# Kernel tuning notes

Measured on AMD Instinct MI355X. Metric: run time of the kernel, lower is better.

## Reference

```python
import jax, jax.numpy as jnp
import numpy as np

NUM_HEADS = 4

def setup_inputs() -> dict:
    key = jax.random.key(0)
    ks = jax.random.split(key, 5)
    B, T, F, C = 2, 128, 256, 256
    # weights scaled ~1/sqrt(C) so softmax is not saturated
    s = 1.0 / np.sqrt(C)
    return {
        "x": jax.random.normal(ks[0], (B, T, F, C), jnp.float32),
        "w_in": jax.random.normal(ks[1], (3 * C, C), jnp.float32) * s,
        "b_in": jax.random.normal(ks[2], (3 * C,), jnp.float32) * 0.01,
        "w_out": jax.random.normal(ks[3], (C, C), jnp.float32) * s,
        "b_out": jax.random.normal(ks[4], (C,), jnp.float32) * 0.01,
        "band": 16,
    }

def reference(x, w_in, b_in, w_out, b_out, band):
    B, T, F, C = x.shape
    H = NUM_HEADS
    D = C // H
    x2 = x.reshape(B * T, F, C)  # attention over frequency, independent per (B,T)
    qkv = x2 @ w_in.T + b_in  # [BT, F, 3C]
    q, k, v = jnp.split(qkv, 3, axis=-1)
    def heads(t):
        return t.reshape(B * T, F, H, D).transpose(0, 2, 1, 3)  # [BT, H, F, D]
    q, k, v = heads(q), heads(k), heads(v)
    scores = jnp.einsum('bhid,bhjd->bhij', q, k) / jnp.sqrt(jnp.asarray(D, x.dtype))
    i = jnp.arange(F)[:, None]
    j = jnp.arange(F)[None, :]
    keep = jnp.abs(i - j) <= band  # banded locality mask [F, F]
    scores = jnp.where(keep, scores, -jnp.inf)
    attn = jax.nn.softmax(scores, axis=-1)
    out = jnp.einsum('bhij,bhjd->bhid', attn, v)  # [BT, H, F, D]
    out = out.transpose(0, 2, 1, 3).reshape(B * T, F, C)
    y = out @ w_out.T + b_out
    return y.reshape(B, T, F, C)
```

## Files before the change

### kernel.cpp

```cpp
#include <hip/hip_runtime.h>
#include <hip/hip_bf16.h>
#include <cstdint>

typedef unsigned int u32;
typedef __attribute__((ext_vector_type(8))) __bf16 bf16x8;
typedef __attribute__((ext_vector_type(4))) float f32x4;
typedef __attribute__((ext_vector_type(2))) _Float16 half2_t;
typedef __attribute__((ext_vector_type(4))) _Float16 half4;
typedef __attribute__((ext_vector_type(2))) __fp16 fp16x2;

#define BT_N 256
#define F_N 256
#define C_N 256
#define H_N 4
#define D_N 64
#define TC_N 768
#define M_N (BT_N * F_N)
#define VT_ST 268

__device__ __forceinline__ ushort f2bf(float f) {
  u32 u = __float_as_uint(f);
  u32 r = (u + 0x7fffu + ((u >> 16) & 1u)) >> 16;
  return (ushort)r;
}

__device__ __forceinline__ u32 pkbf(float a, float b) {
  return (u32)f2bf(a) | ((u32)f2bf(b) << 16);
}

__device__ __forceinline__ void gload_lds16(const ushort* g, ushort* l) {
  __builtin_amdgcn_global_load_lds(
      (const __attribute__((address_space(1))) u32*)g,
      (__attribute__((address_space(3))) u32*)l, 16, 0, 0);
}

__global__ __launch_bounds__(256) void cvt2_f32_bf16_k(
    const float* __restrict__ s0, ushort* __restrict__ d0, int n0,
    const float* __restrict__ s1, ushort* __restrict__ d1, int n1) {
  int idx = blockIdx.x * 256 + threadIdx.x;
  int stride = gridDim.x * 256;
  for (int i = idx; i < n0 + n1; i += stride) {
    const float4* s = (i < n0) ? ((const float4*)s0 + i) : ((const float4*)s1 + (i - n0));
    ushort* d = (i < n0) ? (d0 + (size_t)i * 4) : (d1 + (size_t)(i - n0) * 4);
    float4 v = *s;
    *(uint2*)d = make_uint2(pkbf(v.x, v.y), pkbf(v.z, v.w));
  }
}

template <bool AF32, typename OutT>
__global__ __launch_bounds__(256, 2) void gemm_bt(
    const void* __restrict__ Ap, const ushort* __restrict__ Bp,
    const float* __restrict__ bias, OutT* __restrict__ Cp,
    int N, int NTN, int nwg8) {
  constexpr bool F32OUT = (sizeof(OutT) == 4);
  constexpr int SMEM_BYTES = F32OUT ? 67584 : 65536;
  __shared__ char smem[SMEM_BYTES];
  ushort* smemH = (ushort*)smem;

  const int tid = threadIdx.x;
  const int lane = tid & 63;
  const int wid = tid >> 6;
  const int wr = wid >> 1, wc = wid & 1;
  const int l15 = lane & 15, l4 = lane >> 4;
  const int b = blockIdx.x;
  const int bid = (b & 7) * nwg8 + (b >> 3);
  const int tm = bid / NTN;
  const int tn = bid - tm * NTN;
  const int rowBase = tm * 128, colBase = tn * 128;

  f32x4 acc[4][4] = {};

  const int ar = (tid >> 3);
  const int c8 = tid & 7;
  const int akk = ((c8 ^ (ar & 7)) << 3);
  const ushort* gB = Bp + (size_t)(colBase + ar) * 256 + akk;
  const ushort* gAh = (const ushort*)Ap + (size_t)(rowBase + ar) * 256 + akk;
  const float* gAf = (const float*)Ap + (size_t)(rowBase + ar) * 256 + c8 * 8;

  float4 a0[4], a1[4];

#define STAGE_B(buf, k0)                                                      \
  {                                                                           \
    ushort* Bs_ = smemH + 16384 + (buf) * 8192;                               \
    _Pragma("unroll") for (int c = 0; c < 4; ++c)                             \
      gload_lds16(gB + (size_t)(c * 32) * 256 + (k0),                         \
                  Bs_ + (size_t)(c * 256 + (wid << 6)) * 8);                  \
  }
#define STAGE_A16(buf, k0)                                                    \
  {                                                                           \
    ushort* As_ = smemH + (buf) * 8192;                                       \
    _Pragma("unroll") for (int c = 0; c < 4; ++c)                             \
      gload_lds16(gAh + (size_t)(c * 32) * 256 + (k0),                        \
                  As_ + (size_t)(c * 256 + (wid << 6)) * 8);                  \
  }
#define LOAD_AF(k0)                                                           \
  {                                                                           \
    _Pragma("unroll") for (int c = 0; c < 4; ++c) {                           \
      const float* ga = gAf + (size_t)(c * 32) * 256 + (k0);                  \
      a0[c] = *(const float4*)ga;                                             \
      a1[c] = *(const float4*)(ga + 4);                                       \
    }                                                                         \
  }
#define WRITE_AF(buf)                                                         \
  {                                                                           \
    ushort* As_ = smemH + (buf) * 8192;                                       \
    _Pragma("unroll") for (int c = 0; c < 4; ++c) {                           \
      int row = ar + 32 * c;                                                  \
      u32 p0 = pkbf(a0[c].x, a0[c].y), p1 = pkbf(a0[c].z, a0[c].w);           \
      u32 p2 = pkbf(a1[c].x, a1[c].y), p3 = pkbf(a1[c].z, a1[c].w);           \
      *(uint4*)(As_ + row * 64 + ((c8 ^ (ar & 7)) * 8)) =                     \
          make_uint4(p0, p1, p2, p3);                                         \
    }                                                                         \
  }

  if constexpr (AF32) {
    LOAD_AF(0);
    STAGE_B(0, 0);
    WRITE_AF(0);
  } else {
    STAGE_A16(0, 0);
    STAGE_B(0, 0);
  }

  int cur = 0;
#pragma unroll
  for (int t = 0; t < 4; ++t) {
    __syncthreads();
    if (t < 3) {
      if constexpr (AF32) { LOAD_AF((t + 1) * 64); }
      else { STAGE_A16(cur ^ 1, (t + 1) * 64); }
      STAGE_B(cur ^ 1, (t + 1) * 64);
    }
    const ushort* As_ = smemH + cur * 8192;
    const ushort* Bs_ = smemH + 16384 + cur * 8192;
#pragma unroll
    for (int kk = 0; kk < 2; ++kk) {
      bf16x8 af[4];
      bf16x8 bfr[4];
#pragma unroll
      for (int i2 = 0; i2 < 4; ++i2) {
        int row = wr * 64 + i2 * 16 + l15;
        af[i2] = *(const bf16x8*)(As_ + row * 64 + (((kk * 4 + l4) ^ (l15 & 7)) * 8));
      }
#pragma unroll
      for (int j2 = 0; j2 < 4; ++j2) {
        int row = wc * 64 + j2 * 16 + l15;
        bfr[j2] = *(const bf16x8*)(Bs_ + row * 64 + (((kk * 4 + l4) ^ (l15 & 7)) * 8));
      }
#pragma unroll
      for (int i2 = 0; i2 < 4; ++i2)
#pragma unroll
        for (int j2 = 0; j2 < 4; ++j2)
          acc[i2][j2] = __builtin_amdgcn_mfma_f32_16x16x32_bf16(
              af[i2], bfr[j2], acc[i2][j2], 0, 0, 0);
    }
    if constexpr (AF32) {
      if (t < 3) WRITE_AF(cur ^ 1);
    }
    cur ^= 1;
  }
#undef STAGE_B
#undef STAGE_A16
#undef LOAD_AF
#undef WRITE_AF

  __syncthreads();
  if constexpr (F32OUT) {
    float* eb = (float*)smem;
#pragma unroll
    for (int j2 = 0; j2 < 4; ++j2) {
      float bv = bias[colBase + wc * 64 + j2 * 16 + l15];
#pragma unroll
      for (int i2 = 0; i2 < 4; ++i2)
#pragma unroll
        for (int r = 0; r < 4; ++r)
          eb[(wr * 64 + i2 * 16 + l4 * 4 + r) * 132 + wc * 64 + j2 * 16 + l15] =
              acc[i2][j2][r] + bv;
    }
    __syncthreads();
#pragma unroll
    for (int i = 0; i < 32; ++i) {
      int row = wid * 32 + i;
      uint2 d = *(const uint2*)((const u32*)eb + row * 132 + lane * 2);
      *(uint2*)((float*)Cp + (size_t)(rowBase + row) * N + colBase + lane * 2) = d;
    }
  } else {
    ushort* eb = smemH;
#pragma unroll
    for (int j2 = 0; j2 < 4; ++j2) {
      float bv = bias[colBase + wc * 64 + j2 * 16 + l15];
#pragma unroll
      for (int i2 = 0; i2 < 4; ++i2)
#pragma unroll
        for (int r = 0; r < 4; ++r) {
          _Float16 h = (_Float16)(acc[i2][j2][r] + bv);
          eb[(wr * 64 + i2 * 16 + l4 * 4 + r) * 136 + wc * 64 + j2 * 16 + l15] =
              __builtin_bit_cast(ushort, h);
        }
    }
    __syncthreads();
#pragma unroll
    for (int i = 0; i < 16; ++i) {
      int row = wid * 32 + 2 * i + (lane >> 5);
      int hl = lane & 31;
      uint2 d = *(const uint2*)(eb + row * 136 + hl * 4);
      *(uint2*)((_Float16*)Cp + (size_t)(rowBase + row) * N + colBase + hl * 4) = d;
    }
  }
}

__global__ __launch_bounds__(256) void attn_mfma(
    const _Float16* __restrict__ qkv, ushort* __restrict__ aout) {
  __shared__ ushort smem[18432 + 64 * VT_ST];
  const int tid = threadIdx.x;
  const int bt = blockIdx.x >> 2;
  const int h = blockIdx.x & 3;
  const _Float16* base = qkv + (size_t)bt * 256 * 768 + h * 64;
  ushort* klds = smem;
  ushort* vlds = smem + 18432;

  {
    const int r0 = tid >> 3, c8 = tid & 7;
#pragma unroll
    for (int p = 0; p < 8; ++p) {
      int j = p * 32 + r0;
      const uint4 k4 = *(const uint4*)(base + (size_t)j * 768 + 256 + c8 * 8);
      *(uint4*)(klds + j * 72 + c8 * 8) = k4;
      const uint4 v4 = *(const uint4*)(base + (size_t)j * 768 + 512 + c8 * 8);
      const ushort* vh = (const ushort*)&v4;
      ushort* vtp = vlds + (c8 * 8) * VT_ST + j;
#pragma unroll
      for (int i = 0; i < 8; ++i) vtp[i * VT_ST] = vh[i];
    }
  }

  const int w = tid >> 6, lane = tid & 63;
  const int l15 = lane & 15, g = lane >> 4, g4 = g * 4;

  uint2 qf0[4], qf1[4], qf2[4], qf3[4];
  {
    const uint2* q0 = (const uint2*)(base + (size_t)(w * 64 + 0 * 16 + l15) * 768 + g4);
    const uint2* q1 = (const uint2*)(base + (size_t)(w * 64 + 1 * 16 + l15) * 768 + g4);
    const uint2* q2 = (const uint2*)(base + (size_t)(w * 64 + 2 * 16 + l15) * 768 + g4);
    const uint2* q3 = (const uint2*)(base + (size_t)(w * 64 + 3 * 16 + l15) * 768 + g4);
#pragma unroll
    for (int ks = 0; ks < 4; ++ks) {
      qf0[ks] = q0[ks * 4]; qf1[ks] = q1[ks * 4];
      qf2[ks] = q2[ks * 4]; qf3[ks] = q3[ks * 4];
    }
  }

  u32 bb = 0;
#pragma unroll
  for (int jt = 0; jt < 3; ++jt)
#pragma unroll
    for (int r = 0; r < 4; ++r) {
      int d = 16 * jt + g4 + r - 16 - l15;
      if (d >= -16 && d <= 16) bb |= 1u << (jt * 4 + r);
    }

  __syncthreads();

  const float SC = 0.18033688f;

#pragma unroll
  for (int rt = 0; rt < 4; ++rt) {
    const int R0 = w * 64 + rt * 16;
    const int Jc = R0 - 16;
    const uint2* qf = (rt == 0) ? qf0 : (rt == 1) ? qf1 : (rt == 2) ? qf2 : qf3;

    f32x4 st[3] = {};
#pragma unroll
    for (int jt = 0; jt < 3; ++jt) {
      int krow = Jc + 16 * jt + l15;
      krow = krow < 0 ? 0 : (krow > 255 ? 255 : krow);
      const ushort* kp = klds + krow * 72 + g4;
#pragma unroll
      for (int ks = 0; ks < 4; ++ks) {
        uint2 kf = *(const uint2*)(kp + ks * 16);
        st[jt] = __builtin_amdgcn_mfma_f32_16x16x16f16(
            __builtin_bit_cast(half4, kf), __builtin_bit_cast(half4, qf[ks]),
            st[jt], 0, 0, 0);
      }
    }

    float l_acc = 0.f;
    float pp[3][4];
#pragma unroll
    for (int jt = 0; jt < 3; ++jt)
#pragma unroll
      for (int r = 0; r < 4; ++r) {
        int jg = Jc + 16 * jt + g4 + r;
        bool keep = (((bb >> (jt * 4 + r)) & 1u) != 0) && (jg >= 0) && (jg < 256);
        float pv = keep ? __builtin_amdgcn_exp2f(st[jt][r] * SC) : 0.f;
        pp[jt][r] = pv;
        l_acc += pv;
      }
    l_acc += __shfl_xor(l_acc, 16, 64);
    l_acc += __shfl_xor(l_acc, 32, 64);
    const float inv = 1.f / l_acc;

    uint2 pf[3];
#pragma unroll
    for (int jt = 0; jt < 3; ++jt) {
      fp16x2 a = __builtin_amdgcn_cvt_pkrtz(pp[jt][0] * inv, pp[jt][1] * inv);
      fp16x2 c = __builtin_amdgcn_cvt_pkrtz(pp[jt][2] * inv, pp[jt][3] * inv);
      pf[jt].x = __builtin_bit_cast(u32, a);
      pf[jt].y = __builtin_bit_cast(u32, c);
    }

    f32x4 ot[4] = {};
#pragma unroll
    for (int kt = 0; kt < 3; ++kt) {
      int jb = Jc + 16 * kt + g4;
      jb = jb < 0 ? 0 : (jb > 252 ? 252 : jb);
#pragma unroll
      for (int mt = 0; mt < 4; ++mt) {
        uint2 vfr = *(const uint2*)(vlds + (16 * mt + l15) * VT_ST + jb);
        ot[mt] = __builtin_amdgcn_mfma_f32_16x16x16f16(
            __builtin_bit_cast(half4, vfr), __builtin_bit_cast(half4, pf[kt]),
            ot[mt], 0, 0, 0);
      }
    }

    ushort* orow = aout + (size_t)(bt * 256 + R0 + l15) * 256 + h * 64 + g4;
#pragma unroll
    for (int mt = 0; mt < 4; ++mt) {
      u32 lo = (u32)f2bf(ot[mt][0]) | ((u32)f2bf(ot[mt][1]) << 16);
      u32 hi = (u32)f2bf(ot[mt][2]) | ((u32)f2bf(ot[mt][3]) << 16);
      *(uint2*)(orow + mt * 16) = make_uint2(lo, hi);
    }
  }
}

extern "C" void kernel_launch(void* const* d_in, const int* in_sizes, int n_in,
                              void* d_out, int out_size, void* d_ws, size_t ws_size,
                              hipStream_t stream) {
  const float* x = (const float*)d_in[0];
  const float* w_in = (const float*)d_in[1];
  const float* b_in = (const float*)d_in[2];
  const float* w_out = (const float*)d_in[3];
  const float* b_out = (const float*)d_in[4];
  float* y = (float*)d_out;

  char* ws = (char*)d_ws;
  const size_t qkv_bytes = (size_t)M_N * TC_N * 2;
  _Float16* qkv = (_Float16*)ws;
  ushort* attn = (ushort*)(ws + qkv_bytes);
  ushort* winb = attn + (size_t)M_N * C_N;
  ushort* woutb = winb + TC_N * C_N;

  cvt2_f32_bf16_k<<<256, 256, 0, stream>>>(w_in, winb, TC_N * C_N / 4,
                                           w_out, woutb, C_N * C_N / 4);

  gemm_bt<true, _Float16><<<(M_N / 128) * (TC_N / 128), 256, 0, stream>>>(
      x, winb, b_in, qkv, TC_N, TC_N / 128, (M_N / 128) * (TC_N / 128) / 8);

  attn_mfma<<<BT_N * H_N, 256, 0, stream>>>(qkv, attn);

  gemm_bt<false, float><<<(M_N / 128) * (C_N / 128), 256, 0, stream>>>(
      attn, woutb, b_out, y, C_N, C_N / 128, (M_N / 128) * (C_N / 128) / 8);
}
```

Before: 114.9 us.

## Add dedicated QKV GEMM keeping full-K x rows in registers

Replaces the generic tiled QKV projection with a kernel where each block owns 64 rows of x, loads and converts the full K=256 row slice to bf16 once into registers, and then loops over all six 128-column weight tiles, streaming weights through double-buffered LDS. This removes the redundant re-reading and re-conversion of fp32 x for each of the six N tiles, cutting global traffic on the largest input. In exchange each block does a longer serial loop with high register use (64 bf16x8 A fragments), which may lower occupancy, and the epilogue now writes fp16 output directly from MFMA layout without LDS staging.

```diff
diff --git a/kernel.cpp b/kernel.cpp
--- a/kernel.cpp
+++ b/kernel.cpp
@@ -47,6 +47,100 @@
   }
 }
 
+__global__ __launch_bounds__(256) void gemm_qkv(
+    const float* __restrict__ x, const ushort* __restrict__ wb,
+    const float* __restrict__ bias, _Float16* __restrict__ qkv, int nwg8) {
+  __shared__ ushort Bs[2][128 * 64];
+
+  const int tid = threadIdx.x;
+  const int lane = tid & 63;
+  const int wid = tid >> 6;
+  const int wr = wid >> 1, wc = wid & 1;
+  const int l15 = lane & 15, g = lane >> 4;
+  const int b = blockIdx.x;
+  const int bid = (b & 7) * nwg8 + (b >> 3);
+  const int rowBase = bid * 64;
+
+  bf16x8 af[2][8];
+#pragma unroll
+  for (int i2 = 0; i2 < 2; ++i2) {
+    const float* xr = x + (size_t)(rowBase + wr * 32 + i2 * 16 + l15) * 256 + g * 8;
+#pragma unroll
+    for (int ks = 0; ks < 8; ++ks) {
+      float4 f0 = *(const float4*)(xr + ks * 32);
+      float4 f1 = *(const float4*)(xr + ks * 32 + 4);
+      u32 p0 = pkbf(f0.x, f0.y), p1 = pkbf(f0.z, f0.w);
+      u32 p2 = pkbf(f1.x, f1.y), p3 = pkbf(f1.z, f1.w);
+      uint4 pk = make_uint4(p0, p1, p2, p3);
+      af[i2][ks] = __builtin_bit_cast(bf16x8, pk);
+    }
+  }
+
+  const int sr = tid >> 3;
+  const int sc = tid & 7;
+#define STAGE_B(buf, nt, kt)                                                  \
+  {                                                                           \
+    ushort* B_ = Bs[buf];                                                     \
+    _Pragma("unroll") for (int p = 0; p < 4; ++p) {                           \
+      int r = p * 32 + sr;                                                    \
+      const ushort* gb = wb + (size_t)((nt) * 128 + r) * 256 + (kt) * 64 +    \
+                         ((sc ^ (r & 7)) << 3);                               \
+      gload_lds16(gb, B_ + (size_t)(p * 256 + tid) * 8);                      \
+    }                                                                         \
+  }
+
+  f32x4 acc[2][4] = {};
+  STAGE_B(0, 0, 0);
+
+#pragma unroll
+  for (int nt = 0; nt < 6; ++nt) {
+#pragma unroll
+    for (int kt = 0; kt < 4; ++kt) {
+      const int s = nt * 4 + kt;
+      __syncthreads();
+      if (s < 23) {
+        const int nt2 = (s + 1) >> 2, kt2 = (s + 1) & 3;
+        STAGE_B((s + 1) & 1, nt2, kt2);
+      }
+      const ushort* B_ = Bs[s & 1];
+#pragma unroll
+      for (int kk = 0; kk < 2; ++kk) {
+        bf16x8 bfr[4];
+#pragma unroll
+        for (int j2 = 0; j2 < 4; ++j2) {
+          int row = wc * 64 + j2 * 16 + l15;
+          bfr[j2] = *(const bf16x8*)(B_ + row * 64 + (((kk * 4 + g) ^ (l15 & 7)) * 8));
+        }
+#pragma unroll
+        for (int i2 = 0; i2 < 2; ++i2)
+#pragma unroll
+          for (int j2 = 0; j2 < 4; ++j2)
+            acc[i2][j2] = __builtin_amdgcn_mfma_f32_16x16x32_bf16(
+                bfr[j2], af[i2][kt * 2 + kk], acc[i2][j2], 0, 0, 0);
+      }
+      if (kt == 3) {
+#pragma unroll
+        for (int j2 = 0; j2 < 4; ++j2) {
+          int col = nt * 128 + wc * 64 + j2 * 16 + g * 4;
+          float4 bv = *(const float4*)(bias + col);
+#pragma unroll
+          for (int i2 = 0; i2 < 2; ++i2) {
+            int row = rowBase + wr * 32 + i2 * 16 + l15;
+            fp16x2 lo = __builtin_amdgcn_cvt_pkrtz(acc[i2][j2][0] + bv.x,
+                                                   acc[i2][j2][1] + bv.y);
+            fp16x2 hi = __builtin_amdgcn_cvt_pkrtz(acc[i2][j2][2] + bv.z,
+                                                   acc[i2][j2][3] + bv.w);
+            *(uint2*)(qkv + (size_t)row * 768 + col) =
+                make_uint2(__builtin_bit_cast(u32, lo), __builtin_bit_cast(u32, hi));
+            acc[i2][j2] = f32x4{0.f, 0.f, 0.f, 0.f};
+          }
+        }
+      }
+    }
+  }
+#undef STAGE_B
+}
+
 template <bool AF32, typename OutT>
 __global__ __launch_bounds__(256, 2) void gemm_bt(
     const void* __restrict__ Ap, const ushort* __restrict__ Bp,
@@ -75,9 +169,6 @@
   const int akk = ((c8 ^ (ar & 7)) << 3);
   const ushort* gB = Bp + (size_t)(colBase + ar) * 256 + akk;
   const ushort* gAh = (const ushort*)Ap + (size_t)(rowBase + ar) * 256 + akk;
-  const float* gAf = (const float*)Ap + (size_t)(rowBase + ar) * 256 + c8 * 8;
-
-  float4 a0[4], a1[4];
 
 #define STAGE_B(buf, k0)                                                      \
   {                                                                           \
@@ -93,42 +184,16 @@
       gload_lds16(gAh + (size_t)(c * 32) * 256 + (k0),                        \
                   As_ + (size_t)(c * 256 + (wid << 6)) * 8);                  \
   }
-#define LOAD_AF(k0)                                                           \
-  {                                                                           \
-    _Pragma("unroll") for (int c = 0; c < 4; ++c) {                           \
-      const float* ga = gAf + (size_t)(c * 32) * 256 + (k0);                  \
-      a0[c] = *(const float4*)ga;                                             \
-      a1[c] = *(const float4*)(ga + 4);                                       \
-    }                                                                         \
-  }
-#define WRITE_AF(buf)                                                         \
-  {                                                                           \
-    ushort* As_ = smemH + (buf) * 8192;                                       \
-    _Pragma("unroll") for (int c = 0; c < 4; ++c) {                           \
-      int row = ar + 32 * c;                                                  \
-      u32 p0 = pkbf(a0[c].x, a0[c].y), p1 = pkbf(a0[c].z, a0[c].w);           \
-      u32 p2 = pkbf(a1[c].x, a1[c].y), p3 = pkbf(a1[c].z, a1[c].w);           \
-      *(uint4*)(As_ + row * 64 + ((c8 ^ (ar & 7)) * 8)) =                     \
-          make_uint4(p0, p1, p2, p3);                                         \
-    }                                                                         \
-  }
-
-  if constexpr (AF32) {
-    LOAD_AF(0);
-    STAGE_B(0, 0);
-    WRITE_AF(0);
-  } else {
-    STAGE_A16(0, 0);
-    STAGE_B(0, 0);
-  }
+
+  STAGE_A16(0, 0);
+  STAGE_B(0, 0);
 
   int cur = 0;
 #pragma unroll
   for (int t = 0; t < 4; ++t) {
     __syncthreads();
     if (t < 3) {
-      if constexpr (AF32) { LOAD_AF((t + 1) * 64); }
-      else { STAGE_A16(cur ^ 1, (t + 1) * 64); }
+      STAGE_A16(cur ^ 1, (t + 1) * 64);
       STAGE_B(cur ^ 1, (t + 1) * 64);
     }
     const ushort* As_ = smemH + cur * 8192;
@@ -154,15 +219,10 @@
           acc[i2][j2] = __builtin_amdgcn_mfma_f32_16x16x32_bf16(
               af[i2], bfr[j2], acc[i2][j2], 0, 0, 0);
     }
-    if constexpr (AF32) {
-      if (t < 3) WRITE_AF(cur ^ 1);
-    }
     cur ^= 1;
   }
 #undef STAGE_B
 #undef STAGE_A16
-#undef LOAD_AF
-#undef WRITE_AF
 
   __syncthreads();
   if constexpr (F32OUT) {
@@ -353,8 +413,7 @@
   cvt2_f32_bf16_k<<<256, 256, 0, stream>>>(w_in, winb, TC_N * C_N / 4,
                                            w_out, woutb, C_N * C_N / 4);
 
-  gemm_bt<true, _Float16><<<(M_N / 128) * (TC_N / 128), 256, 0, stream>>>(
-      x, winb, b_in, qkv, TC_N, TC_N / 128, (M_N / 128) * (TC_N / 128) / 8);
+  gemm_qkv<<<M_N / 64, 256, 0, stream>>>(x, winb, b_in, qkv, (M_N / 64) / 8);
 
   attn_mfma<<<BT_N * H_N, 256, 0, stream>>>(qkv, attn);
 
```

Result: no change. 116.1 us (+1.1%).
